# Optimization experiments

Hardware: AMD Instinct MI355X
Metric: run time of the kernel (lower is better)

## Reference

```python
import jax, jax.numpy as jnp
import numpy as np

V, D, N, S = 100000, 256, 8192, 20
H = D  # hidden size == feat_dim (nn.LSTM(feat_dim, feat_dim))


def setup_inputs() -> dict:
    key = jax.random.key(0)
    ks = jax.random.split(key, 8)
    sc = 1.0 / np.sqrt(H)  # PyTorch LSTM default init scale
    return {
        "emb": jax.random.normal(ks[0], (V, D), jnp.float32),
        "w_ih_f": jax.random.normal(ks[1], (4 * H, D), jnp.float32) * sc,
        "w_hh_f": jax.random.normal(ks[2], (4 * H, H), jnp.float32) * sc,
        "b_f": jax.random.normal(ks[3], (4 * H,), jnp.float32) * sc,
        "w_ih_b": jax.random.normal(ks[4], (4 * H, D), jnp.float32) * sc,
        "w_hh_b": jax.random.normal(ks[5], (4 * H, H), jnp.float32) * sc,
        "b_b": jax.random.normal(ks[6], (4 * H,), jnp.float32) * sc,
        "neigh_idx": jax.random.randint(ks[7], (N, S), 0, V, dtype=jnp.int64),
    }


def _lstm_dir(x, w_ih, w_hh, b):
    """Batched unidirectional LSTM. x: [N, S, D] -> hidden states [N, S, H].
    PyTorch gate order: i, f, g, o."""
    h_dim = w_hh.shape[1]
    # precompute input contribution for all steps: [N, S, 4H]
    xg = jnp.einsum('nsd,gd->nsg', x, w_ih) + b

    def step(carry, xt):
        h, c = carry
        g = xt + h @ w_hh.T
        i, f, gg, o = jnp.split(g, 4, axis=-1)
        c = jax.nn.sigmoid(f) * c + jax.nn.sigmoid(i) * jnp.tanh(gg)
        h = jax.nn.sigmoid(o) * jnp.tanh(c)
        return (h, c), h

    n = x.shape[0]
    init = (jnp.zeros((n, h_dim), x.dtype), jnp.zeros((n, h_dim), x.dtype))
    _, hs = jax.lax.scan(step, init, jnp.swapaxes(xg, 0, 1))  # [S, N, H]
    return jnp.swapaxes(hs, 0, 1)


def reference(emb, w_ih_f, w_hh_f, b_f, w_ih_b, w_hh_b, b_b, neigh_idx):
    x = emb[neigh_idx]  # gather neighbor embeddings: [N, S, D]
    hf = _lstm_dir(x, w_ih_f, w_hh_f, b_f)                      # [N, S, H]
    hb = _lstm_dir(x[:, ::-1, :], w_ih_b, w_hh_b, b_b)[:, ::-1, :]
    h = jnp.concatenate([hf, hb], axis=-1)  # [N, S, 2H]
    summed = h.sum(axis=1)                  # sum over time: [N, 2H]
    # faithful to original: torch.mean over the 1-D summed vector -> scalar
    # broadcast into the full output row
    row = summed.mean(axis=-1, keepdims=True)  # [N, 1]
    return jnp.broadcast_to(row, summed.shape)  # [N, 2H]
```

## Files before the change

### kernel.cpp

```cpp
#include <hip/hip_runtime.h>

#define NN 8192
#define SS 20
#define DD 256
#define RGATE 1024
#define KKD 512

typedef __attribute__((ext_vector_type(8))) short short8;
typedef __attribute__((ext_vector_type(4))) float f32x4;

__device__ __forceinline__ unsigned short f2bf(float f) {
    unsigned int u = __float_as_uint(f);
    u += 0x7FFFu + ((u >> 16) & 1u);
    return (unsigned short)(u >> 16);
}

__device__ __forceinline__ void async_copy16(const void* g, void* l) {
    __builtin_amdgcn_global_load_lds(
        (const __attribute__((address_space(1))) void*)g,
        (__attribute__((address_space(3))) void*)l, 16, 0, 0);
}

__device__ __forceinline__ float sigm(float x) { return 1.0f / (1.0f + __expf(-x)); }
__device__ __forceinline__ float tanh_(float x) { return 2.0f / (1.0f + __expf(-2.0f * x)) - 1.0f; }

__global__ void convert_w(const float* __restrict__ wihf, const float* __restrict__ whhf,
                          const float* __restrict__ bf,   const float* __restrict__ wihb,
                          const float* __restrict__ whhb, const float* __restrict__ bb,
                          unsigned short* __restrict__ Wcat, float* __restrict__ bperm) {
    const int idx = blockIdx.x * 256 + threadIdx.x;
    const int dir = idx >> 19;
    const int rem = idx & ((1 << 19) - 1);
    const int rp  = rem >> 9;
    const int k   = rem & 511;
    const int j   = rp >> 2, gi = rp & 3;
    const int r   = gi * 256 + j;
    const float* wih = dir ? wihb : wihf;
    const float* whh = dir ? whhb : whhf;
    const float v = (k < 256) ? wih[r * 256 + k] : whh[r * 256 + (k - 256)];
    Wcat[idx] = f2bf(v);
    if (k == 0) {
        const float* b = dir ? bb : bf;
        bperm[dir * 1024 + rp] = b[r];
    }
}

__global__ __launch_bounds__(256) void gather_x(const float* __restrict__ emb,
                                                const int* __restrict__ idx,
                                                unsigned short* __restrict__ X) {
    const int w = threadIdx.x >> 6, lane = threadIdx.x & 63;
    #pragma unroll 4
    for (int i = 0; i < 16; ++i) {
        const int rid = (blockIdx.x * 16 + i) * 4 + w;
        const int n = rid / SS, t = rid - n * SS;
        const int row = idx[rid];
        const float4 v = ((const float4*)(emb + (size_t)row * DD))[lane];
        ushort4 o;
        o.x = f2bf(v.x); o.y = f2bf(v.y); o.z = f2bf(v.z); o.w = f2bf(v.w);
        ((ushort4*)(X + ((size_t)t * NN + n) * DD))[lane] = o;
    }
}

__global__ __launch_bounds__(512, 2) void lstm_step(
    const unsigned short* __restrict__ X,
    const unsigned short* __restrict__ Wcat,
    const float* __restrict__ bperm,
    unsigned short* __restrict__ hping,
    float* __restrict__ cstate,
    float* __restrict__ hsum,
    int s) {
    const int b     = blockIdx.x;
    const int dir   = b & 1;
    const int nblk  = (b >> 3) & 3;
    const int mslab = (((b & 7) >> 1) << 3) | (b >> 5);
    const int m0    = mslab * 256;
    const int n0    = nblk * 256;

    const int t = dir ? (SS - 1 - s) : s;
    const unsigned short* Xt    = X + (size_t)t * NN * DD;
    const unsigned short* hprev = hping + ((size_t)((s & 1) * 2 + dir)) * NN * 256;
    unsigned short*       hnext = hping + ((size_t)((((s + 1) & 1) * 2) + dir)) * NN * 256;
    const unsigned short* W     = Wcat + (size_t)dir * RGATE * KKD;
    const float*          bp    = bperm + dir * RGATE;
    float*                cdir  = cstate + (size_t)dir * NN * 256;

    __shared__ __align__(16) char smem[65536];

    const int tid  = threadIdx.x;
    const int lane = tid & 63;
    const int w    = tid >> 6;
    const int wm   = w >> 1, wn = w & 1;
    const int quad = lane >> 4, l15 = lane & 15;
    const int jq   = lane & 3,  rl  = lane >> 2;

    const int srow  = lane >> 2;
    const int gsegl = (lane & 3) ^ ((lane >> 3) & 3);

    auto stage = [&](int r, int buf) {
        const int k0 = (r & 7) * 32;
        const unsigned short* Asrc = (r < 8) ? Xt : hprev;
        char* Ad = smem + buf * 16384;
        char* Bd = smem + 32768 + buf * 16384;
        #pragma unroll
        for (int i = 0; i < 2; ++i) {
            const int lr = w * 32 + i * 16 + srow;
            async_copy16(Asrc + (size_t)(m0 + lr) * DD + k0 + gsegl * 8,
                         (void*)(Ad + (w * 32 + i * 16) * 64));
            async_copy16(W + (size_t)(n0 + lr) * KKD + r * 32 + gsegl * 8,
                         (void*)(Bd + (w * 32 + i * 16) * 64));
        }
    };

    f32x4 acc[4][8];
    #pragma unroll
    for (int i = 0; i < 4; ++i)
        #pragma unroll
        for (int j = 0; j < 8; ++j) acc[i][j] = f32x4{0.f, 0.f, 0.f, 0.f};

    stage(0, 0);
    __syncthreads();

    const int sA = (quad ^ ((l15 >> 1) & 3)) * 16;

    for (int r = 0; r < 16; ++r) {
        if (r < 15) stage(r + 1, (r + 1) & 1);
        const char* Ab = smem + (r & 1) * 16384;
        const char* Bb = smem + 32768 + (r & 1) * 16384;
        short8 af[4], bf[8];
        #pragma unroll
        for (int mt = 0; mt < 4; ++mt)
            af[mt] = *(const short8*)(Ab + (wm * 64 + mt * 16 + l15) * 64 + sA);
        #pragma unroll
        for (int nt = 0; nt < 8; ++nt)
            bf[nt] = *(const short8*)(Bb + (wn * 128 + nt * 16 + l15) * 64 + sA);
        #pragma unroll
        for (int mt = 0; mt < 4; ++mt)
            #pragma unroll
            for (int nt = 0; nt < 8; ++nt)
                acc[mt][nt] = __builtin_amdgcn_mfma_f32_16x16x32_bf16(
                    af[mt], bf[nt], acc[mt][nt], 0, 0, 0);
        __syncthreads();
    }

    float* my = (float*)smem + w * 1088;
    float hs[4] = {0.f, 0.f, 0.f, 0.f};

    #pragma unroll
    for (int half = 0; half < 2; ++half) {
        const int j0 = nblk * 64 + wn * 32 + half * 16 + jq * 4;
        f32x4 bias4[4];
        #pragma unroll
        for (int jj = 0; jj < 4; ++jj)
            bias4[jj] = *(const f32x4*)(bp + 4 * (j0 + jj));
        #pragma unroll
        for (int mt = 0; mt < 4; ++mt) {
            #pragma unroll
            for (int nt = 0; nt < 4; ++nt) {
                const int ntg = half * 4 + nt;
                #pragma unroll
                for (int v = 0; v < 4; ++v)
                    my[(quad * 4 + v) * 68 + nt * 16 + l15] = acc[mt][ntg][v];
            }
            asm volatile("s_waitcnt lgkmcnt(0)" ::: "memory");
            const int mg = m0 + wm * 64 + mt * 16 + rl;
            float* cptr = cdir + (size_t)mg * 256 + j0;
            f32x4 cold = *(const f32x4*)cptr;
            f32x4 cnew;
            ushort4 hp;
            float lsum = 0.f;
            #pragma unroll
            for (int jj = 0; jj < 4; ++jj) {
                f32x4 g  = *(const f32x4*)(my + rl * 68 + (jq * 4 + jj) * 4);
                f32x4 bb = bias4[jj];
                const float gi = sigm(g.x + bb.x);
                const float gf = sigm(g.y + bb.y);
                const float gg = tanh_(g.z + bb.z);
                const float go = sigm(g.w + bb.w);
                const float cn = gf * cold[jj] + gi * gg;
                cnew[jj] = cn;
                const float hv = go * tanh_(cn);
                lsum += hv;
                ((unsigned short*)&hp)[jj] = f2bf(hv);
            }
            *(f32x4*)cptr = cnew;
            *(ushort4*)(hnext + (size_t)mg * 256 + j0) = hp;
            hs[mt] += lsum;
        }
    }

    #pragma unroll
    for (int mt = 0; mt < 4; ++mt) {
        float v = hs[mt];
        v += __shfl_xor(v, 1);
        v += __shfl_xor(v, 2);
        if (jq == 0) atomicAdd(&hsum[m0 + wm * 64 + mt * 16 + rl], v);
    }
}

__global__ void bcast_out(const float* __restrict__ hsum, float* __restrict__ out) {
    const int n = blockIdx.x;
    const float v = hsum[n] * (1.0f / 512.0f);
    float2 p; p.x = v; p.y = v;
    ((float2*)(out + (size_t)n * 512))[threadIdx.x] = p;
}

extern "C" void kernel_launch(void* const* d_in, const int* in_sizes, int n_in,
                              void* d_out, int out_size, void* d_ws, size_t ws_size,
                              hipStream_t stream) {
    const float* emb  = (const float*)d_in[0];
    const float* wihf = (const float*)d_in[1];
    const float* whhf = (const float*)d_in[2];
    const float* bf   = (const float*)d_in[3];
    const float* wihb = (const float*)d_in[4];
    const float* whhb = (const float*)d_in[5];
    const float* bb   = (const float*)d_in[6];
    const int*   idx  = (const int*)d_in[7];
    float* out = (float*)d_out;

    char* ws = (char*)d_ws;
    unsigned short* X     = (unsigned short*)(ws);
    unsigned short* Wcat  = (unsigned short*)(ws + 83886080);
    float*          bperm = (float*)(ws + 85983232);
    unsigned short* hping = (unsigned short*)(ws + 85991424);
    float*          cst   = (float*)(ws + 102768640);
    float*          hsum  = (float*)(ws + 119545856);

    hipMemsetAsync(hping, 0, 8388608, stream);
    hipMemsetAsync(cst, 0, 16777216 + 32768, stream);

    convert_w<<<4096, 256, 0, stream>>>(wihf, whhf, bf, wihb, whhb, bb, Wcat, bperm);
    gather_x<<<2560, 256, 0, stream>>>(emb, idx, X);
    for (int s = 0; s < SS; ++s)
        lstm_step<<<256, 512, 0, stream>>>(X, Wcat, bperm, hping, cst, hsum, s);
    bcast_out<<<NN, 256, 0, stream>>>(hsum, out);
}
```

Measured before the change: 811.0 us.

## Triple-buffer LDS staging with explicit vmcnt waits in LSTM step GEMM

Moves the K-loop of the per-timestep gate GEMM from double to triple buffering in LDS (96KB). Each round waits only on the older outstanding async copies (s_waitcnt vmcnt(4)) before a raw s_barrier, so two stages are in flight while MFMAs run. The goal is to hide global-to-LDS latency behind compute. In exchange, the larger LDS footprint may cut occupancy, and the hand-written waitcnt/barrier sequence is fragile with respect to compiler scheduling.

```diff
diff --git a/kernel.cpp b/kernel.cpp
--- a/kernel.cpp
+++ b/kernel.cpp
@@ -84,7 +84,7 @@
     const float*          bp    = bperm + dir * RGATE;
     float*                cdir  = cstate + (size_t)dir * NN * 256;
 
-    __shared__ __align__(16) char smem[65536];
+    __shared__ __align__(16) char smem[98304];
 
     const int tid  = threadIdx.x;
     const int lane = tid & 63;
@@ -96,17 +96,17 @@
     const int srow  = lane >> 2;
     const int gsegl = (lane & 3) ^ ((lane >> 3) & 3);
 
-    auto stage = [&](int r, int buf) {
-        const int k0 = (r & 7) * 32;
-        const unsigned short* Asrc = (r < 8) ? Xt : hprev;
+    auto stage = [&](int rr, int buf) {
+        const int k0 = (rr & 7) * 32;
+        const unsigned short* Asrc = (rr < 8) ? Xt : hprev;
         char* Ad = smem + buf * 16384;
-        char* Bd = smem + 32768 + buf * 16384;
+        char* Bd = smem + 49152 + buf * 16384;
         #pragma unroll
         for (int i = 0; i < 2; ++i) {
             const int lr = w * 32 + i * 16 + srow;
             async_copy16(Asrc + (size_t)(m0 + lr) * DD + k0 + gsegl * 8,
                          (void*)(Ad + (w * 32 + i * 16) * 64));
-            async_copy16(W + (size_t)(n0 + lr) * KKD + r * 32 + gsegl * 8,
+            async_copy16(W + (size_t)(n0 + lr) * KKD + rr * 32 + gsegl * 8,
                          (void*)(Bd + (w * 32 + i * 16) * 64));
         }
     };
@@ -117,29 +117,46 @@
         #pragma unroll
         for (int j = 0; j < 8; ++j) acc[i][j] = f32x4{0.f, 0.f, 0.f, 0.f};
 
-    stage(0, 0);
-    __syncthreads();
-
     const int sA = (quad ^ ((l15 >> 1) & 3)) * 16;
 
-    for (int r = 0; r < 16; ++r) {
-        if (r < 15) stage(r + 1, (r + 1) & 1);
-        const char* Ab = smem + (r & 1) * 16384;
-        const char* Bb = smem + 32768 + (r & 1) * 16384;
-        short8 af[4], bf[8];
+    auto krnd = [&](int cb) {
+        const char* Ab = smem + cb * 16384;
+        const char* Bb = smem + 49152 + cb * 16384;
+        short8 af[4], bfr[8];
         #pragma unroll
         for (int mt = 0; mt < 4; ++mt)
             af[mt] = *(const short8*)(Ab + (wm * 64 + mt * 16 + l15) * 64 + sA);
         #pragma unroll
         for (int nt = 0; nt < 8; ++nt)
-            bf[nt] = *(const short8*)(Bb + (wn * 128 + nt * 16 + l15) * 64 + sA);
+            bfr[nt] = *(const short8*)(Bb + (wn * 128 + nt * 16 + l15) * 64 + sA);
         #pragma unroll
         for (int mt = 0; mt < 4; ++mt)
             #pragma unroll
             for (int nt = 0; nt < 8; ++nt)
                 acc[mt][nt] = __builtin_amdgcn_mfma_f32_16x16x32_bf16(
-                    af[mt], bf[nt], acc[mt][nt], 0, 0, 0);
-        __syncthreads();
+                    af[mt], bfr[nt], acc[mt][nt], 0, 0, 0);
+    };
+
+    stage(0, 0);
+    stage(1, 1);
+    {
+        int cb = 0, sb = 2;
+        #pragma unroll
+        for (int r = 0; r < 14; ++r) {
+            asm volatile("s_waitcnt vmcnt(4)" ::: "memory");
+            asm volatile("s_barrier" ::: "memory");
+            krnd(cb);
+            stage(r + 2, sb);
+            cb = (cb == 2) ? 0 : cb + 1;
+            sb = (sb == 2) ? 0 : sb + 1;
+        }
+        asm volatile("s_waitcnt vmcnt(4)" ::: "memory");
+        asm volatile("s_barrier" ::: "memory");
+        krnd(2);
+        asm volatile("s_waitcnt vmcnt(0)" ::: "memory");
+        asm volatile("s_barrier" ::: "memory");
+        krnd(0);
+        asm volatile("s_barrier" ::: "memory");
     }
 
     float* my = (float*)smem + w * 1088;
```

Measured after the change: 745.6 us. -8.1%, faster.
